# Kernel tuning notes

Measured on AMD Instinct MI355X. Metric: run time of the kernel, lower is better.

The kernel has to match this reference:

```python
import jax, jax.numpy as jnp
import numpy as np

# Module hyperparameters (init_kwargs)
H, W, C = 80, 80, 6
N = H * W
THETA_ALPHA = 8.0   # bilateral spatial bandwidth
THETA_BETA = 0.15   # bilateral color bandwidth (feature_map in [0,1))
THETA_GAMMA = 3.0   # spatial-only bandwidth
NUM_ITER = 5


def setup_inputs() -> dict:
    key = jax.random.key(0)
    k1, k2, k3, k4, k5, k6 = jax.random.split(key, 6)
    eye = jnp.eye(C, dtype=jnp.float32)
    return {
        'unary_potentials': jax.random.normal(k1, (1, H, W, C), jnp.float32),
        'feature_map': jax.random.uniform(k2, (H, W, 3), jnp.float32),
        # Potts init (-I) / identity inits, perturbed so grads are nontrivial
        'compatibility_matrix': -eye + 0.05 * jax.random.normal(k3, (C, C), jnp.float32),
        'local_global_potential': eye + 0.05 * jax.random.normal(k4, (C, C), jnp.float32),
        'spatial_ker_weights': eye + 0.05 * jax.random.normal(k5, (C, C), jnp.float32),
        'bilateral_ker_weights': eye + 0.05 * jax.random.normal(k6, (C, C), jnp.float32),
    }


def _sqdist(a):
    # a: [N, d] -> pairwise squared distances [N, N]
    s = jnp.sum(a * a, axis=-1)
    return s[:, None] + s[None, :] - 2.0 * (a @ a.T)


def _kernels(feature_map):
    # Exact dense Gaussian kernels (the math the permutohedral filter approximates)
    yy, xx = jnp.meshgrid(jnp.arange(H, dtype=jnp.float32),
                          jnp.arange(W, dtype=jnp.float32), indexing='ij')
    pos = jnp.stack([yy.ravel(), xx.ravel()], axis=-1)       # [N, 2]
    d2p = _sqdist(pos)                                       # [N, N]
    feat = feature_map.reshape(N, 3)
    d2f = _sqdist(feat)                                      # [N, N]
    Ks = jnp.exp(-d2p / (2.0 * THETA_GAMMA ** 2))            # spatial kernel
    Kb = jnp.exp(-d2p / (2.0 * THETA_ALPHA ** 2) - d2f / (2.0 * THETA_BETA ** 2))
    return Ks, Kb


def _forward(unary_potentials, feature_map, compatibility_matrix,
             local_global_potential, spatial_ker_weights, bilateral_ker_weights):
    Ks, Kb = _kernels(feature_map)
    norm_s = jnp.sum(Ks, axis=1)  # = high_dim_filter(ones), per-pixel normalizer [N]
    norm_b = jnp.sum(Kb, axis=1)
    unary = jnp.transpose(unary_potentials[0], (2, 0, 1)).reshape(C, N)  # [C, N]

    def message(sm):  # sm: [C, N]
        sp = spatial_ker_weights @ ((sm @ Ks) / norm_s)   # kernels symmetric
        bl = bilateral_ker_weights @ ((sm @ Kb) / norm_b)
        return sp + bl

    def elbo_for_label(lg_col):  # lg_col = local_global_potential[:, y], shape [C]
        q = unary
        sm = jax.nn.softmax(q, axis=0)
        for _ in range(NUM_ITER):
            sm = jax.nn.softmax(q, axis=0)
            pairwise = compatibility_matrix @ message(sm)
            # einsum('ij,jkl->ikl', W, onehot_y) == W[:, y] broadcast over pixels
            q = unary + lg_col[:, None] - pairwise
        # ELBO uses sm from the last iteration (softmax of the pre-update q)
        unary_term = jnp.sum(sm * unary)
        lg_term = jnp.dot(lg_col, jnp.sum(sm, axis=1))
        pairwise_term = -jnp.sum(message(sm) * sm)
        entropy = -jnp.sum(sm * jnp.log(sm + 1e-10))
        return unary_term + lg_term + entropy + pairwise_term

    lg_cols = local_global_potential.T  # row y is column y of W
    return jax.vmap(elbo_for_label)(lg_cols)  # [C] elbos, one per label y


def reference(unary_potentials, feature_map, compatibility_matrix,
              local_global_potential, spatial_ker_weights, bilateral_ker_weights):
    return _forward(unary_potentials, feature_map, compatibility_matrix,
                    local_global_potential, spatial_ker_weights, bilateral_ker_weights)
```

## Files before the change

### kernel.cpp

```cpp
#include <hip/hip_runtime.h>
#include <hip/hip_bf16.h>
#include <math.h>

#define HH 80
#define WW 80
#define NPIX 6400
#define CC 36
#define CCP 48
#define NC 6
#define NUM_ITER 5
#define LN2 0.6931471805599453

typedef __attribute__((ext_vector_type(8))) short bfrag;
typedef __attribute__((ext_vector_type(4))) float f32x4;

__device__ __constant__ const float kCg = (float)(-1.0 / (18.0 * LN2));
__device__ __constant__ const float kSA = 0.08838834764831845f;
__device__ __constant__ const float kSB = 5.663898078577187f;

__device__ inline unsigned short f2bf(float f) {
    unsigned u = __builtin_bit_cast(unsigned, f);
    unsigned r = (u + 0x7FFFu + ((u >> 16) & 1u)) >> 16;
    return (unsigned short)r;
}

__global__ __launch_bounds__(256) void k_init(const float* __restrict__ unary,
                                              const float* __restrict__ feat,
                                              float* __restrict__ sm,
                                              unsigned short* __restrict__ smbT,
                                              float* __restrict__ pf,
                                              float* __restrict__ norm_s) {
    int i = blockIdx.x * 256 + threadIdx.x;
    if (i >= NPIX) return;
    int y = i / WW, x = i - y * WW;
    float Sy = 0.f, Sx = 0.f;
    for (int t = 0; t < 80; t++) {
        float dy = (float)(y - t), dx = (float)(x - t);
        Sy += __builtin_amdgcn_exp2f(kCg * dy * dy);
        Sx += __builtin_amdgcn_exp2f(kCg * dx * dx);
    }
    norm_s[i] = Sy * Sx;
    pf[0 * NPIX + i] = kSA * (float)y;
    pf[1 * NPIX + i] = kSA * (float)x;
    pf[2 * NPIX + i] = kSB * feat[i * 3 + 0];
    pf[3 * NPIX + i] = kSB * feat[i * 3 + 1];
    pf[4 * NPIX + i] = kSB * feat[i * 3 + 2];
    float v[NC], mx = -1e30f;
#pragma unroll
    for (int c = 0; c < NC; c++) { v[c] = unary[i * NC + c]; mx = fmaxf(mx, v[c]); }
    float sum = 0.f;
#pragma unroll
    for (int c = 0; c < NC; c++) { v[c] = __expf(v[c] - mx); sum += v[c]; }
    float inv = 1.f / sum;
#pragma unroll
    for (int l = 0; l < NC; l++)
#pragma unroll
        for (int c = 0; c < NC; c++) {
            float s = v[c] * inv;
            sm[(size_t)i * CC + l * NC + c] = s;
            smbT[(size_t)(l * NC + c) * NPIX + i] = f2bf(s);
        }
    smbT[(size_t)36 * NPIX + i] = 0x3F80;
#pragma unroll
    for (int cc = 37; cc < CCP; cc++) smbT[(size_t)cc * NPIX + i] = 0;
}

__global__ __launch_bounds__(256) void k_bil_convx(const unsigned short* __restrict__ smbT,
                                                   const float* __restrict__ pf,
                                                   const float* __restrict__ sm,
                                                   float* __restrict__ part_b,
                                                   float* __restrict__ tmpx,
                                                   int js, int bilblocks) {
    __shared__ float g[80];
    int tid = threadIdx.x;
    int bid = blockIdx.x;
    if (bid < bilblocks) {
        int s = bid / 50, ib = bid - s * 50;
        int slice = NPIX / js;
        int ntiles = slice >> 5;
        int j00 = s * slice;
        int wv = tid >> 6, lane = tid & 63;
        int r = lane & 15, gq = lane >> 4;
        int it0 = ib * 128 + wv * 32;
        int iA = it0 + r, iB = iA + 16;

        const float* py = pf + 0 * NPIX;
        const float* px = pf + 1 * NPIX;
        const float* p0 = pf + 2 * NPIX;
        const float* p1 = pf + 3 * NPIX;
        const float* p2 = pf + 4 * NPIX;

        float yA = py[iA], xA = px[iA], fA0 = p0[iA], fA1 = p1[iA], fA2 = p2[iA];
        float yB = py[iB], xB = px[iB], fB0 = p0[iB], fB1 = p1[iB], fB2 = p2[iB];

        f32x4 accA[3], accB[3];
#pragma unroll
        for (int t = 0; t < 3; t++) {
            accA[t] = (f32x4){0.f, 0.f, 0.f, 0.f};
            accB[t] = (f32x4){0.f, 0.f, 0.f, 0.f};
        }

        for (int jt = 0; jt < ntiles; jt++) {
            int jb = j00 + jt * 32 + 8 * gq;
            f32x4 yj0 = *(const f32x4*)(py + jb), yj1 = *(const f32x4*)(py + jb + 4);
            f32x4 xj0 = *(const f32x4*)(px + jb), xj1 = *(const f32x4*)(px + jb + 4);
            f32x4 c00 = *(const f32x4*)(p0 + jb), c01 = *(const f32x4*)(p0 + jb + 4);
            f32x4 c10 = *(const f32x4*)(p1 + jb), c11 = *(const f32x4*)(p1 + jb + 4);
            f32x4 c20 = *(const f32x4*)(p2 + jb), c21 = *(const f32x4*)(p2 + jb + 4);
            bfrag Bf[3];
#pragma unroll
            for (int t = 0; t < 3; t++)
                Bf[t] = *(const bfrag*)(smbT + (size_t)(16 * t + r) * NPIX + jb);

            float wA[8], wB[8];
#pragma unroll
            for (int e = 0; e < 8; e++) {
                float yj = (e < 4) ? yj0[e & 3] : yj1[e & 3];
                float xj = (e < 4) ? xj0[e & 3] : xj1[e & 3];
                float u0 = (e < 4) ? c00[e & 3] : c01[e & 3];
                float u1 = (e < 4) ? c10[e & 3] : c11[e & 3];
                float u2 = (e < 4) ? c20[e & 3] : c21[e & 3];
                float dy = yA - yj, dx = xA - xj;
                float d0 = fA0 - u0, d1 = fA1 - u1, d2 = fA2 - u2;
                float a = dy * dy;
                a = fmaf(dx, dx, a); a = fmaf(d0, d0, a);
                a = fmaf(d1, d1, a); a = fmaf(d2, d2, a);
                wA[e] = __builtin_amdgcn_exp2f(-a);
                dy = yB - yj; dx = xB - xj;
                d0 = fB0 - u0; d1 = fB1 - u1; d2 = fB2 - u2;
                a = dy * dy;
                a = fmaf(dx, dx, a); a = fmaf(d0, d0, a);
                a = fmaf(d1, d1, a); a = fmaf(d2, d2, a);
                wB[e] = __builtin_amdgcn_exp2f(-a);
            }
            union { unsigned u[4]; bfrag v; } Am, Bm;
#pragma unroll
            for (int m = 0; m < 4; m++) {
                asm("v_cvt_pk_bf16_f32 %0, %1, %2" : "=v"(Am.u[m]) : "v"(wA[2 * m]), "v"(wA[2 * m + 1]));
                asm("v_cvt_pk_bf16_f32 %0, %1, %2" : "=v"(Bm.u[m]) : "v"(wB[2 * m]), "v"(wB[2 * m + 1]));
            }
#pragma unroll
            for (int t = 0; t < 3; t++) {
                accA[t] = __builtin_amdgcn_mfma_f32_16x16x32_bf16(Am.v, Bf[t], accA[t], 0, 0, 0);
                accB[t] = __builtin_amdgcn_mfma_f32_16x16x32_bf16(Bm.v, Bf[t], accB[t], 0, 0, 0);
            }
        }
#pragma unroll
        for (int t = 0; t < 3; t++)
#pragma unroll
            for (int dreg = 0; dreg < 4; dreg++) {
                int irow = it0 + 4 * gq + dreg;
                part_b[((size_t)s * NPIX + irow) * CCP + 16 * t + r] = accA[t][dreg];
                part_b[((size_t)s * NPIX + irow + 16) * CCP + 16 * t + r] = accB[t][dreg];
            }
    } else {
        if (tid < 80) { float d = (float)tid; g[tid] = __builtin_amdgcn_exp2f(kCg * d * d); }
        __syncthreads();
        int t = (bid - bilblocks) * 256 + tid;
        int cc = t % CC;
        int x = (t / CC) % WW;
        int y = t / (CC * WW);
        const float* row = sm + (size_t)(y * WW) * CC + cc;
        float a = 0.f;
        for (int xp = 0; xp < WW; xp++) a = fmaf(g[abs(x - xp)], row[(size_t)xp * CC], a);
        tmpx[t] = a;
    }
}

__global__ __launch_bounds__(256) void k_convy(const float* __restrict__ in,
                                               float* __restrict__ out) {
    __shared__ float g[80];
    int tid = threadIdx.x;
    if (tid < 80) { float d = (float)tid; g[tid] = __builtin_amdgcn_exp2f(kCg * d * d); }
    __syncthreads();
    int t = blockIdx.x * 256 + tid;
    int cc = t % CC;
    int x = (t / CC) % WW;
    int y = t / (CC * WW);
    float a = 0.f;
    for (int yp = 0; yp < HH; yp++)
        a = fmaf(g[abs(y - yp)], in[(size_t)(yp * WW + x) * CC + cc], a);
    out[t] = a;
}

template <bool NORM, bool LAST>
__global__ __launch_bounds__(256) void k_update(const float* __restrict__ part_b,
                                                const float* __restrict__ filt_s,
                                                const float* __restrict__ norm_s,
                                                float* __restrict__ norm_b,
                                                const float* __restrict__ unary,
                                                const float* __restrict__ SW,
                                                const float* __restrict__ BW,
                                                const float* __restrict__ CM,
                                                const float* __restrict__ LG,
                                                float* __restrict__ sm,
                                                unsigned short* __restrict__ smbT,
                                                float* __restrict__ msg,
                                                int js) {
    __shared__ float sSW[36], sBW[36], sCM[36], sLG[36];
    int tid = threadIdx.x;
    if (tid < 36) { sSW[tid] = SW[tid]; sBW[tid] = BW[tid]; sCM[tid] = CM[tid]; sLG[tid] = LG[tid]; }
    __syncthreads();
    int t = blockIdx.x * 256 + tid;
    if (t >= NPIX * NC) return;
    int n = t / NC, l = t - n * NC;
    float invs = 1.f / norm_s[n];
    float invb;
    float fb[NC];
#pragma unroll
    for (int c = 0; c < NC; c++) fb[c] = 0.f;
    float nb = 0.f;
    for (int s = 0; s < js; s++) {
        const float* pp = part_b + ((size_t)s * NPIX + n) * CCP;
#pragma unroll
        for (int c = 0; c < NC; c++) fb[c] += pp[l * NC + c];
        if (NORM) nb += pp[36];
    }
    if (NORM) {
        norm_b[n] = nb;
        invb = 1.f / nb;
    } else {
        invb = 1.f / norm_b[n];
    }
    float fs[NC];
    const float* fsp = filt_s + (size_t)n * CC + l * NC;
#pragma unroll
    for (int c = 0; c < NC; c++) { fs[c] = fsp[c] * invs; fb[c] *= invb; }
    float m[NC];
#pragma unroll
    for (int c = 0; c < NC; c++) {
        float a = 0.f;
#pragma unroll
        for (int cp = 0; cp < NC; cp++)
            a += sSW[c * NC + cp] * fs[cp] + sBW[c * NC + cp] * fb[cp];
        m[c] = a;
    }
    float* mp = msg + (size_t)n * CC + l * NC;
#pragma unroll
    for (int c = 0; c < NC; c++) mp[c] = m[c];
    const float* up = unary + (size_t)n * NC;
    float qv[NC], mxq = -1e30f;
#pragma unroll
    for (int c = 0; c < NC; c++) {
        float pw = 0.f;
#pragma unroll
        for (int cp = 0; cp < NC; cp++) pw += sCM[c * NC + cp] * m[cp];
        qv[c] = up[c] + sLG[c * NC + l] - pw;
        mxq = fmaxf(mxq, qv[c]);
    }
    if (!LAST) {
        float e[NC], ssum = 0.f;
#pragma unroll
        for (int c = 0; c < NC; c++) { e[c] = __expf(qv[c] - mxq); ssum += e[c]; }
        float inv = 1.f / ssum;
        float* sp = sm + (size_t)n * CC + l * NC;
#pragma unroll
        for (int c = 0; c < NC; c++) {
            float sv = e[c] * inv;
            sp[c] = sv;
            smbT[(size_t)(l * NC + c) * NPIX + n] = f2bf(sv);
        }
    }
}

__global__ __launch_bounds__(256) void k_elbo(const float* __restrict__ sm,
                                              const float* __restrict__ msg,
                                              const float* __restrict__ unary,
                                              const float* __restrict__ LG,
                                              float* __restrict__ out) {
    __shared__ float red[256];
    int l = blockIdx.y;
    int n = blockIdx.x * 256 + threadIdx.x;
    float v = 0.f;
    if (n < NPIX) {
        const float* sp = sm + (size_t)n * CC + l * NC;
        const float* mp = msg + (size_t)n * CC + l * NC;
        const float* up = unary + (size_t)n * NC;
#pragma unroll
        for (int c = 0; c < NC; c++) {
            float s = sp[c];
            v += s * (up[c] + LG[c * NC + l] - logf(s + 1e-10f) - mp[c]);
        }
    }
    red[threadIdx.x] = v;
    __syncthreads();
    for (int off = 128; off > 0; off >>= 1) {
        if (threadIdx.x < off) red[threadIdx.x] += red[threadIdx.x + off];
        __syncthreads();
    }
    if (threadIdx.x == 0) atomicAdd(&out[l], red[0]);
}

extern "C" void kernel_launch(void* const* d_in, const int* in_sizes, int n_in,
                              void* d_out, int out_size, void* d_ws, size_t ws_size,
                              hipStream_t stream) {
    const float* unary = (const float*)d_in[0];
    const float* feat  = (const float*)d_in[1];
    const float* CM    = (const float*)d_in[2];
    const float* LG    = (const float*)d_in[3];
    const float* SW    = (const float*)d_in[4];
    const float* BW    = (const float*)d_in[5];
    float* out = (float*)d_out;

    const size_t fixed_f = (size_t)175 * NPIX;
    int js = 20;
    if (ws_size < (fixed_f + (size_t)js * NPIX * CCP) * 4) js = 10;
    if (ws_size < (fixed_f + (size_t)js * NPIX * CCP) * 4) js = 5;
    if (ws_size < (fixed_f + (size_t)js * NPIX * CCP) * 4) js = 4;

    float* ws = (float*)d_ws;
    float* norm_s  = ws;
    float* norm_b  = norm_s + NPIX;
    float* pf      = norm_b + NPIX;
    float* sm      = pf + (size_t)5 * NPIX;
    float* tmpx    = sm + (size_t)NPIX * CC;
    float* filt_s  = tmpx + (size_t)NPIX * CC;
    float* msg     = filt_s + (size_t)NPIX * CC;
    unsigned short* smbT = (unsigned short*)(msg + (size_t)NPIX * CC);
    float* part_b  = (float*)(smbT + (size_t)CCP * NPIX);

    int bilblocks = 50 * js;

    k_init<<<25, 256, 0, stream>>>(unary, feat, sm, smbT, pf, norm_s);

    for (int it = 0; it < NUM_ITER; it++) {
        k_bil_convx<<<bilblocks + 900, 256, 0, stream>>>(smbT, pf, sm, part_b, tmpx,
                                                         js, bilblocks);
        k_convy<<<900, 256, 0, stream>>>(tmpx, filt_s);
        if (it == 0)
            k_update<true, false><<<150, 256, 0, stream>>>(part_b, filt_s, norm_s, norm_b,
                                                           unary, SW, BW, CM, LG,
                                                           sm, smbT, msg, js);
        else if (it < NUM_ITER - 1)
            k_update<false, false><<<150, 256, 0, stream>>>(part_b, filt_s, norm_s, norm_b,
                                                            unary, SW, BW, CM, LG,
                                                            sm, smbT, msg, js);
        else
            k_update<false, true><<<150, 256, 0, stream>>>(part_b, filt_s, norm_s, norm_b,
                                                           unary, SW, BW, CM, LG,
                                                           sm, smbT, msg, js);
    }

    hipMemsetAsync(out, 0, out_size * sizeof(float), stream);
    k_elbo<<<dim3(25, NC), 256, 0, stream>>>(sm, msg, unary, LG, out);
}
```

Baseline: 331.7 us.

## Compute spatial filter inside bilateral MFMA kernel and fuse ELBO into last update

New measurement: 282.3 us. 1.18x faster.

```diff
diff --git a/kernel.cpp b/kernel.cpp
--- a/kernel.cpp
+++ b/kernel.cpp
@@ -9,14 +9,16 @@
 #define CCP 48
 #define NC 6
 #define NUM_ITER 5
-#define LN2 0.6931471805599453
+#define JS 10
+#define SLICE (NPIX / JS)
+#define JTILES (SLICE / 32)
 
 typedef __attribute__((ext_vector_type(8))) short bfrag;
 typedef __attribute__((ext_vector_type(4))) float f32x4;
 
-__device__ __constant__ const float kCg = (float)(-1.0 / (18.0 * LN2));
 __device__ __constant__ const float kSA = 0.08838834764831845f;
 __device__ __constant__ const float kSB = 5.663898078577187f;
+__device__ __constant__ const float kRS = 7.11111111f;
 
 __device__ inline unsigned short f2bf(float f) {
     unsigned u = __builtin_bit_cast(unsigned, f);
@@ -28,18 +30,10 @@
                                               const float* __restrict__ feat,
                                               float* __restrict__ sm,
                                               unsigned short* __restrict__ smbT,
-                                              float* __restrict__ pf,
-                                              float* __restrict__ norm_s) {
+                                              float* __restrict__ pf) {
     int i = blockIdx.x * 256 + threadIdx.x;
     if (i >= NPIX) return;
     int y = i / WW, x = i - y * WW;
-    float Sy = 0.f, Sx = 0.f;
-    for (int t = 0; t < 80; t++) {
-        float dy = (float)(y - t), dx = (float)(x - t);
-        Sy += __builtin_amdgcn_exp2f(kCg * dy * dy);
-        Sx += __builtin_amdgcn_exp2f(kCg * dx * dx);
-    }
-    norm_s[i] = Sy * Sx;
     pf[0 * NPIX + i] = kSA * (float)y;
     pf[1 * NPIX + i] = kSA * (float)x;
     pf[2 * NPIX + i] = kSB * feat[i * 3 + 0];
@@ -53,141 +47,113 @@
     for (int c = 0; c < NC; c++) { v[c] = __expf(v[c] - mx); sum += v[c]; }
     float inv = 1.f / sum;
 #pragma unroll
-    for (int l = 0; l < NC; l++)
+    for (int l = 0; l < NC; l++) {
 #pragma unroll
         for (int c = 0; c < NC; c++) {
             float s = v[c] * inv;
             sm[(size_t)i * CC + l * NC + c] = s;
-            smbT[(size_t)(l * NC + c) * NPIX + i] = f2bf(s);
-        }
-    smbT[(size_t)36 * NPIX + i] = 0x3F80;
-#pragma unroll
-    for (int cc = 37; cc < CCP; cc++) smbT[(size_t)cc * NPIX + i] = 0;
-}
-
-__global__ __launch_bounds__(256) void k_bil_convx(const unsigned short* __restrict__ smbT,
-                                                   const float* __restrict__ pf,
-                                                   const float* __restrict__ sm,
-                                                   float* __restrict__ part_b,
-                                                   float* __restrict__ tmpx,
-                                                   int js, int bilblocks) {
-    __shared__ float g[80];
-    int tid = threadIdx.x;
-    int bid = blockIdx.x;
-    if (bid < bilblocks) {
-        int s = bid / 50, ib = bid - s * 50;
-        int slice = NPIX / js;
-        int ntiles = slice >> 5;
-        int j00 = s * slice;
-        int wv = tid >> 6, lane = tid & 63;
-        int r = lane & 15, gq = lane >> 4;
-        int it0 = ib * 128 + wv * 32;
-        int iA = it0 + r, iB = iA + 16;
-
-        const float* py = pf + 0 * NPIX;
-        const float* px = pf + 1 * NPIX;
-        const float* p0 = pf + 2 * NPIX;
-        const float* p1 = pf + 3 * NPIX;
-        const float* p2 = pf + 4 * NPIX;
-
-        float yA = py[iA], xA = px[iA], fA0 = p0[iA], fA1 = p1[iA], fA2 = p2[iA];
-        float yB = py[iB], xB = px[iB], fB0 = p0[iB], fB1 = p1[iB], fB2 = p2[iB];
-
-        f32x4 accA[3], accB[3];
+            smbT[(size_t)(l * 8 + c) * NPIX + i] = f2bf(s);
+        }
+        smbT[(size_t)(l * 8 + 6) * NPIX + i] = 0x3F80;
+        smbT[(size_t)(l * 8 + 7) * NPIX + i] = 0;
+    }
+}
+
+__global__ __launch_bounds__(256) void k_bil(const unsigned short* __restrict__ smbT,
+                                             const float* __restrict__ pf,
+                                             float* __restrict__ part_b,
+                                             float* __restrict__ part_s) {
+    int tid = threadIdx.x, bid = blockIdx.x;
+    int s = bid / 50, ib = bid - s * 50;
+    int j00 = s * SLICE;
+    int wv = tid >> 6, lane = tid & 63, r = lane & 15, gq = lane >> 4;
+    int it0 = ib * 128 + wv * 32;
+    int iA = it0 + r, iB = iA + 16;
+
+    const float* py = pf;
+    const float* px = pf + NPIX;
+    const float* p0 = pf + 2 * NPIX;
+    const float* p1 = pf + 3 * NPIX;
+    const float* p2 = pf + 4 * NPIX;
+
+    float yA = py[iA], xA = px[iA], fA0 = p0[iA], fA1 = p1[iA], fA2 = p2[iA];
+    float yB = py[iB], xB = px[iB], fB0 = p0[iB], fB1 = p1[iB], fB2 = p2[iB];
+
+    f32x4 aAb[3], aBb[3], aAs[3], aBs[3];
+#pragma unroll
+    for (int t = 0; t < 3; t++) {
+        aAb[t] = (f32x4){0.f, 0.f, 0.f, 0.f};
+        aBb[t] = (f32x4){0.f, 0.f, 0.f, 0.f};
+        aAs[t] = (f32x4){0.f, 0.f, 0.f, 0.f};
+        aBs[t] = (f32x4){0.f, 0.f, 0.f, 0.f};
+    }
+
+    for (int jt = 0; jt < JTILES; jt++) {
+        int jb = j00 + jt * 32 + 8 * gq;
+        f32x4 yj0 = *(const f32x4*)(py + jb), yj1 = *(const f32x4*)(py + jb + 4);
+        f32x4 xj0 = *(const f32x4*)(px + jb), xj1 = *(const f32x4*)(px + jb + 4);
+        f32x4 c00 = *(const f32x4*)(p0 + jb), c01 = *(const f32x4*)(p0 + jb + 4);
+        f32x4 c10 = *(const f32x4*)(p1 + jb), c11 = *(const f32x4*)(p1 + jb + 4);
+        f32x4 c20 = *(const f32x4*)(p2 + jb), c21 = *(const f32x4*)(p2 + jb + 4);
+        bfrag Bf[3];
+#pragma unroll
+        for (int t = 0; t < 3; t++)
+            Bf[t] = *(const bfrag*)(smbT + (size_t)(16 * t + r) * NPIX + jb);
+
+        float wAb[8], wAs[8], wBb[8], wBs[8];
+#pragma unroll
+        for (int e = 0; e < 8; e++) {
+            float yj = (e < 4) ? yj0[e & 3] : yj1[e & 3];
+            float xj = (e < 4) ? xj0[e & 3] : xj1[e & 3];
+            float u0 = (e < 4) ? c00[e & 3] : c01[e & 3];
+            float u1 = (e < 4) ? c10[e & 3] : c11[e & 3];
+            float u2 = (e < 4) ? c20[e & 3] : c21[e & 3];
+            float dy = yA - yj, dx = xA - xj;
+            float sp = dy * dy; sp = fmaf(dx, dx, sp);
+            float d0 = fA0 - u0, d1 = fA1 - u1, d2 = fA2 - u2;
+            float ab = fmaf(d0, d0, sp); ab = fmaf(d1, d1, ab); ab = fmaf(d2, d2, ab);
+            wAb[e] = __builtin_amdgcn_exp2f(-ab);
+            wAs[e] = __builtin_amdgcn_exp2f(-kRS * sp);
+            dy = yB - yj; dx = xB - xj;
+            sp = dy * dy; sp = fmaf(dx, dx, sp);
+            d0 = fB0 - u0; d1 = fB1 - u1; d2 = fB2 - u2;
+            ab = fmaf(d0, d0, sp); ab = fmaf(d1, d1, ab); ab = fmaf(d2, d2, ab);
+            wBb[e] = __builtin_amdgcn_exp2f(-ab);
+            wBs[e] = __builtin_amdgcn_exp2f(-kRS * sp);
+        }
+        union { unsigned u[4]; bfrag v; } Ab, As, Bb, Bs;
+#pragma unroll
+        for (int m = 0; m < 4; m++) {
+            asm("v_cvt_pk_bf16_f32 %0, %1, %2" : "=v"(Ab.u[m]) : "v"(wAb[2 * m]), "v"(wAb[2 * m + 1]));
+            asm("v_cvt_pk_bf16_f32 %0, %1, %2" : "=v"(As.u[m]) : "v"(wAs[2 * m]), "v"(wAs[2 * m + 1]));
+            asm("v_cvt_pk_bf16_f32 %0, %1, %2" : "=v"(Bb.u[m]) : "v"(wBb[2 * m]), "v"(wBb[2 * m + 1]));
+            asm("v_cvt_pk_bf16_f32 %0, %1, %2" : "=v"(Bs.u[m]) : "v"(wBs[2 * m]), "v"(wBs[2 * m + 1]));
+        }
 #pragma unroll
         for (int t = 0; t < 3; t++) {
-            accA[t] = (f32x4){0.f, 0.f, 0.f, 0.f};
-            accB[t] = (f32x4){0.f, 0.f, 0.f, 0.f};
-        }
-
-        for (int jt = 0; jt < ntiles; jt++) {
-            int jb = j00 + jt * 32 + 8 * gq;
-            f32x4 yj0 = *(const f32x4*)(py + jb), yj1 = *(const f32x4*)(py + jb + 4);
-            f32x4 xj0 = *(const f32x4*)(px + jb), xj1 = *(const f32x4*)(px + jb + 4);
-            f32x4 c00 = *(const f32x4*)(p0 + jb), c01 = *(const f32x4*)(p0 + jb + 4);
-            f32x4 c10 = *(const f32x4*)(p1 + jb), c11 = *(const f32x4*)(p1 + jb + 4);
-            f32x4 c20 = *(const f32x4*)(p2 + jb), c21 = *(const f32x4*)(p2 + jb + 4);
-            bfrag Bf[3];
-#pragma unroll
-            for (int t = 0; t < 3; t++)
-                Bf[t] = *(const bfrag*)(smbT + (size_t)(16 * t + r) * NPIX + jb);
-
-            float wA[8], wB[8];
-#pragma unroll
-            for (int e = 0; e < 8; e++) {
-                float yj = (e < 4) ? yj0[e & 3] : yj1[e & 3];
-                float xj = (e < 4) ? xj0[e & 3] : xj1[e & 3];
-                float u0 = (e < 4) ? c00[e & 3] : c01[e & 3];
-                float u1 = (e < 4) ? c10[e & 3] : c11[e & 3];
-                float u2 = (e < 4) ? c20[e & 3] : c21[e & 3];
-                float dy = yA - yj, dx = xA - xj;
-                float d0 = fA0 - u0, d1 = fA1 - u1, d2 = fA2 - u2;
-                float a = dy * dy;
-                a = fmaf(dx, dx, a); a = fmaf(d0, d0, a);
-                a = fmaf(d1, d1, a); a = fmaf(d2, d2, a);
-                wA[e] = __builtin_amdgcn_exp2f(-a);
-                dy = yB - yj; dx = xB - xj;
-                d0 = fB0 - u0; d1 = fB1 - u1; d2 = fB2 - u2;
-                a = dy * dy;
-                a = fmaf(dx, dx, a); a = fmaf(d0, d0, a);
-                a = fmaf(d1, d1, a); a = fmaf(d2, d2, a);
-                wB[e] = __builtin_amdgcn_exp2f(-a);
-            }
-            union { unsigned u[4]; bfrag v; } Am, Bm;
-#pragma unroll
-            for (int m = 0; m < 4; m++) {
-                asm("v_cvt_pk_bf16_f32 %0, %1, %2" : "=v"(Am.u[m]) : "v"(wA[2 * m]), "v"(wA[2 * m + 1]));
-                asm("v_cvt_pk_bf16_f32 %0, %1, %2" : "=v"(Bm.u[m]) : "v"(wB[2 * m]), "v"(wB[2 * m + 1]));
-            }
-#pragma unroll
-            for (int t = 0; t < 3; t++) {
-                accA[t] = __builtin_amdgcn_mfma_f32_16x16x32_bf16(Am.v, Bf[t], accA[t], 0, 0, 0);
-                accB[t] = __builtin_amdgcn_mfma_f32_16x16x32_bf16(Bm.v, Bf[t], accB[t], 0, 0, 0);
-            }
-        }
-#pragma unroll
-        for (int t = 0; t < 3; t++)
-#pragma unroll
-            for (int dreg = 0; dreg < 4; dreg++) {
-                int irow = it0 + 4 * gq + dreg;
-                part_b[((size_t)s * NPIX + irow) * CCP + 16 * t + r] = accA[t][dreg];
-                part_b[((size_t)s * NPIX + irow + 16) * CCP + 16 * t + r] = accB[t][dreg];
-            }
-    } else {
-        if (tid < 80) { float d = (float)tid; g[tid] = __builtin_amdgcn_exp2f(kCg * d * d); }
-        __syncthreads();
-        int t = (bid - bilblocks) * 256 + tid;
-        int cc = t % CC;
-        int x = (t / CC) % WW;
-        int y = t / (CC * WW);
-        const float* row = sm + (size_t)(y * WW) * CC + cc;
-        float a = 0.f;
-        for (int xp = 0; xp < WW; xp++) a = fmaf(g[abs(x - xp)], row[(size_t)xp * CC], a);
-        tmpx[t] = a;
-    }
-}
-
-__global__ __launch_bounds__(256) void k_convy(const float* __restrict__ in,
-                                               float* __restrict__ out) {
-    __shared__ float g[80];
-    int tid = threadIdx.x;
-    if (tid < 80) { float d = (float)tid; g[tid] = __builtin_amdgcn_exp2f(kCg * d * d); }
-    __syncthreads();
-    int t = blockIdx.x * 256 + tid;
-    int cc = t % CC;
-    int x = (t / CC) % WW;
-    int y = t / (CC * WW);
-    float a = 0.f;
-    for (int yp = 0; yp < HH; yp++)
-        a = fmaf(g[abs(y - yp)], in[(size_t)(yp * WW + x) * CC + cc], a);
-    out[t] = a;
-}
-
-template <bool NORM, bool LAST>
+            aAb[t] = __builtin_amdgcn_mfma_f32_16x16x32_bf16(Ab.v, Bf[t], aAb[t], 0, 0, 0);
+            aAs[t] = __builtin_amdgcn_mfma_f32_16x16x32_bf16(As.v, Bf[t], aAs[t], 0, 0, 0);
+            aBb[t] = __builtin_amdgcn_mfma_f32_16x16x32_bf16(Bb.v, Bf[t], aBb[t], 0, 0, 0);
+            aBs[t] = __builtin_amdgcn_mfma_f32_16x16x32_bf16(Bs.v, Bf[t], aBs[t], 0, 0, 0);
+        }
+    }
+#pragma unroll
+    for (int t = 0; t < 3; t++)
+#pragma unroll
+        for (int d = 0; d < 4; d++) {
+            int irow = it0 + 4 * gq + d;
+            size_t o1 = ((size_t)s * NPIX + irow) * CCP + 16 * t + r;
+            size_t o2 = ((size_t)s * NPIX + irow + 16) * CCP + 16 * t + r;
+            part_b[o1] = aAb[t][d];
+            part_b[o2] = aBb[t][d];
+            part_s[o1] = aAs[t][d];
+            part_s[o2] = aBs[t][d];
+        }
+}
+
+template <bool LAST>
 __global__ __launch_bounds__(256) void k_update(const float* __restrict__ part_b,
-                                                const float* __restrict__ filt_s,
-                                                const float* __restrict__ norm_s,
-                                                float* __restrict__ norm_b,
+                                                const float* __restrict__ part_s,
                                                 const float* __restrict__ unary,
                                                 const float* __restrict__ SW,
                                                 const float* __restrict__ BW,
@@ -195,37 +161,33 @@
                                                 const float* __restrict__ LG,
                                                 float* __restrict__ sm,
                                                 unsigned short* __restrict__ smbT,
-                                                float* __restrict__ msg,
-                                                int js) {
+                                                float* __restrict__ out) {
     __shared__ float sSW[36], sBW[36], sCM[36], sLG[36];
+    __shared__ float bins[NC];
     int tid = threadIdx.x;
     if (tid < 36) { sSW[tid] = SW[tid]; sBW[tid] = BW[tid]; sCM[tid] = CM[tid]; sLG[tid] = LG[tid]; }
+    if (LAST && tid < NC) bins[tid] = 0.f;
     __syncthreads();
     int t = blockIdx.x * 256 + tid;
-    if (t >= NPIX * NC) return;
     int n = t / NC, l = t - n * NC;
-    float invs = 1.f / norm_s[n];
-    float invb;
-    float fb[NC];
-#pragma unroll
-    for (int c = 0; c < NC; c++) fb[c] = 0.f;
-    float nb = 0.f;
-    for (int s = 0; s < js; s++) {
-        const float* pp = part_b + ((size_t)s * NPIX + n) * CCP;
-#pragma unroll
-        for (int c = 0; c < NC; c++) fb[c] += pp[l * NC + c];
-        if (NORM) nb += pp[36];
-    }
-    if (NORM) {
-        norm_b[n] = nb;
-        invb = 1.f / nb;
-    } else {
-        invb = 1.f / norm_b[n];
-    }
-    float fs[NC];
-    const float* fsp = filt_s + (size_t)n * CC + l * NC;
-#pragma unroll
-    for (int c = 0; c < NC; c++) { fs[c] = fsp[c] * invs; fb[c] *= invb; }
+
+    float fb[NC], fs[NC], nb = 0.f, ns = 0.f;
+#pragma unroll
+    for (int c = 0; c < NC; c++) { fb[c] = 0.f; fs[c] = 0.f; }
+    for (int s = 0; s < JS; s++) {
+        const float4* pb = (const float4*)(part_b + ((size_t)s * NPIX + n) * CCP + l * 8);
+        const float4* ps = (const float4*)(part_s + ((size_t)s * NPIX + n) * CCP + l * 8);
+        float4 b0 = pb[0], b1 = pb[1];
+        float4 s0 = ps[0], s1 = ps[1];
+        fb[0] += b0.x; fb[1] += b0.y; fb[2] += b0.z; fb[3] += b0.w;
+        fb[4] += b1.x; fb[5] += b1.y; nb += b1.z;
+        fs[0] += s0.x; fs[1] += s0.y; fs[2] += s0.z; fs[3] += s0.w;
+        fs[4] += s1.x; fs[5] += s1.y; ns += s1.z;
+    }
+    float invb = 1.f / nb, invs = 1.f / ns;
+#pragma unroll
+    for (int c = 0; c < NC; c++) { fb[c] *= invb; fs[c] *= invs; }
+
     float m[NC];
 #pragma unroll
     for (int c = 0; c < NC; c++) {
@@ -235,20 +197,17 @@
             a += sSW[c * NC + cp] * fs[cp] + sBW[c * NC + cp] * fb[cp];
         m[c] = a;
     }
-    float* mp = msg + (size_t)n * CC + l * NC;
-#pragma unroll
-    for (int c = 0; c < NC; c++) mp[c] = m[c];
     const float* up = unary + (size_t)n * NC;
-    float qv[NC], mxq = -1e30f;
-#pragma unroll
-    for (int c = 0; c < NC; c++) {
-        float pw = 0.f;
-#pragma unroll
-        for (int cp = 0; cp < NC; cp++) pw += sCM[c * NC + cp] * m[cp];
-        qv[c] = up[c] + sLG[c * NC + l] - pw;
-        mxq = fmaxf(mxq, qv[c]);
-    }
     if (!LAST) {
+        float qv[NC], mxq = -1e30f;
+#pragma unroll
+        for (int c = 0; c < NC; c++) {
+            float pw = 0.f;
+#pragma unroll
+            for (int cp = 0; cp < NC; cp++) pw += sCM[c * NC + cp] * m[cp];
+            qv[c] = up[c] + sLG[c * NC + l] - pw;
+            mxq = fmaxf(mxq, qv[c]);
+        }
         float e[NC], ssum = 0.f;
 #pragma unroll
         for (int c = 0; c < NC; c++) { e[c] = __expf(qv[c] - mxq); ssum += e[c]; }
@@ -258,37 +217,20 @@
         for (int c = 0; c < NC; c++) {
             float sv = e[c] * inv;
             sp[c] = sv;
-            smbT[(size_t)(l * NC + c) * NPIX + n] = f2bf(sv);
-        }
-    }
-}
-
-__global__ __launch_bounds__(256) void k_elbo(const float* __restrict__ sm,
-                                              const float* __restrict__ msg,
-                                              const float* __restrict__ unary,
-                                              const float* __restrict__ LG,
-                                              float* __restrict__ out) {
-    __shared__ float red[256];
-    int l = blockIdx.y;
-    int n = blockIdx.x * 256 + threadIdx.x;
-    float v = 0.f;
-    if (n < NPIX) {
+            smbT[(size_t)(l * 8 + c) * NPIX + n] = f2bf(sv);
+        }
+    } else {
         const float* sp = sm + (size_t)n * CC + l * NC;
-        const float* mp = msg + (size_t)n * CC + l * NC;
-        const float* up = unary + (size_t)n * NC;
-#pragma unroll
-        for (int c = 0; c < NC; c++) {
-            float s = sp[c];
-            v += s * (up[c] + LG[c * NC + l] - logf(s + 1e-10f) - mp[c]);
-        }
-    }
-    red[threadIdx.x] = v;
-    __syncthreads();
-    for (int off = 128; off > 0; off >>= 1) {
-        if (threadIdx.x < off) red[threadIdx.x] += red[threadIdx.x + off];
+        float v = 0.f;
+#pragma unroll
+        for (int c = 0; c < NC; c++) {
+            float sv = sp[c];
+            v += sv * (up[c] + sLG[c * NC + l] - logf(sv + 1e-10f) - m[c]);
+        }
+        atomicAdd(&bins[l], v);
         __syncthreads();
-    }
-    if (threadIdx.x == 0) atomicAdd(&out[l], red[0]);
+        if (tid < NC) atomicAdd(&out[tid], bins[tid]);
+    }
 }
 
 extern "C" void kernel_launch(void* const* d_in, const int* in_sizes, int n_in,
@@ -302,45 +244,23 @@
     const float* BW    = (const float*)d_in[5];
     float* out = (float*)d_out;
 
-    const size_t fixed_f = (size_t)175 * NPIX;
-    int js = 20;
-    if (ws_size < (fixed_f + (size_t)js * NPIX * CCP) * 4) js = 10;
-    if (ws_size < (fixed_f + (size_t)js * NPIX * CCP) * 4) js = 5;
-    if (ws_size < (fixed_f + (size_t)js * NPIX * CCP) * 4) js = 4;
-
     float* ws = (float*)d_ws;
-    float* norm_s  = ws;
-    float* norm_b  = norm_s + NPIX;
-    float* pf      = norm_b + NPIX;
-    float* sm      = pf + (size_t)5 * NPIX;
-    float* tmpx    = sm + (size_t)NPIX * CC;
-    float* filt_s  = tmpx + (size_t)NPIX * CC;
-    float* msg     = filt_s + (size_t)NPIX * CC;
-    unsigned short* smbT = (unsigned short*)(msg + (size_t)NPIX * CC);
-    float* part_b  = (float*)(smbT + (size_t)CCP * NPIX);
-
-    int bilblocks = 50 * js;
-
-    k_init<<<25, 256, 0, stream>>>(unary, feat, sm, smbT, pf, norm_s);
+    float* pf = ws;
+    float* sm = pf + (size_t)5 * NPIX;
+    unsigned short* smbT = (unsigned short*)(sm + (size_t)CC * NPIX);
+    float* part_b = sm + (size_t)(CC + 24) * NPIX;
+    float* part_s = part_b + (size_t)JS * NPIX * CCP;
+
+    hipMemsetAsync(out, 0, out_size * sizeof(float), stream);
+    k_init<<<25, 256, 0, stream>>>(unary, feat, sm, smbT, pf);
 
     for (int it = 0; it < NUM_ITER; it++) {
-        k_bil_convx<<<bilblocks + 900, 256, 0, stream>>>(smbT, pf, sm, part_b, tmpx,
-                                                         js, bilblocks);
-        k_convy<<<900, 256, 0, stream>>>(tmpx, filt_s);
-        if (it == 0)
-            k_update<true, false><<<150, 256, 0, stream>>>(part_b, filt_s, norm_s, norm_b,
-                                                           unary, SW, BW, CM, LG,
-                                                           sm, smbT, msg, js);
-        else if (it < NUM_ITER - 1)
-            k_update<false, false><<<150, 256, 0, stream>>>(part_b, filt_s, norm_s, norm_b,
-                                                            unary, SW, BW, CM, LG,
-                                                            sm, smbT, msg, js);
+        k_bil<<<JS * 50, 256, 0, stream>>>(smbT, pf, part_b, part_s);
+        if (it < NUM_ITER - 1)
+            k_update<false><<<150, 256, 0, stream>>>(part_b, part_s, unary,
+                                                     SW, BW, CM, LG, sm, smbT, out);
         else
-            k_update<false, true><<<150, 256, 0, stream>>>(part_b, filt_s, norm_s, norm_b,
-                                                           unary, SW, BW, CM, LG,
-                                                           sm, smbT, msg, js);
-    }
-
-    hipMemsetAsync(out, 0, out_size * sizeof(float), stream);
-    k_elbo<<<dim3(25, NC), 256, 0, stream>>>(sm, msg, unary, LG, out);
-}
+            k_update<true><<<150, 256, 0, stream>>>(part_b, part_s, unary,
+                                                    SW, BW, CM, LG, sm, smbT, out);
+    }
+}
```
